# Kernel optimization log

Measured on AMD Instinct MI355X. Metric: run time of the kernel, lower is better.

The kernel has to match this reference:

```python
import jax, jax.numpy as jnp
import numpy as np

B, N, DIM = 4, 1024, 512
H, DH = 8, 64
INNER = H * DH
MLP = 2048
EPS = 1e-5


def layernorm(x, g, b):
    m = x.mean(-1, keepdims=True)
    v = ((x - m) ** 2).mean(-1, keepdims=True)
    return (x - m) / jnp.sqrt(v + EPS) * g + b


def setup_inputs() -> dict:
    key = jax.random.key(0)
    ks = jax.random.split(key, 12)
    s = 0.02
    return {
        "q": jax.random.normal(ks[0], (B, N, DIM), jnp.float32),
        "k": jax.random.normal(ks[1], (B, N, DIM), jnp.float32),
        "v": jax.random.normal(ks[2], (B, N, DIM), jnp.float32),
        "Win": jax.random.normal(ks[3], (INNER, DIM), jnp.float32) * s,
        "Wout": jax.random.normal(ks[4], (DIM, INNER), jnp.float32) * s,
        "bout": jnp.zeros((DIM,), jnp.float32),
        "g1": jnp.ones((DIM,), jnp.float32),
        "b1n": jnp.zeros((DIM,), jnp.float32),
        "g2": jnp.ones((DIM,), jnp.float32),
        "b2n": jnp.zeros((DIM,), jnp.float32),
        "Wup": jax.random.normal(ks[5], (MLP, DIM), jnp.float32) * s,
        "bup": jnp.zeros((MLP,), jnp.float32),
        "Wdn": jax.random.normal(ks[6], (DIM, MLP), jnp.float32) * s,
        "bdn": jnp.zeros((DIM,), jnp.float32),
        "wp_W1": jax.random.normal(ks[7], (DH, 2 * DH), jnp.float32) * s,
        "wp_b1": jnp.zeros((DH,), jnp.float32),
        "wp_g": jnp.ones((DH,), jnp.float32),
        "wp_b": jnp.zeros((DH,), jnp.float32),
        "wp_W2": jax.random.normal(ks[8], (3, DH), jnp.float32) * s,
        "wp_b2": jnp.zeros((3,), jnp.float32),
        "num_heads": H,
        "dim_head": DH,
        "mlp_dim": MLP,
    }


def reference(q, k, v, Win, Wout, bout, g1, b1n, g2, b2n, Wup, bup, Wdn, bdn,
              wp_W1, wp_b1, wp_g, wp_b, wp_W2, wp_b2, num_heads, dim_head, mlp_dim):
    b, n, _ = q.shape

    def split_heads(x):  # [b,n,dim] -> [h,b,n,d]
        f = x @ Win.T
        return f.reshape(b, n, num_heads, dim_head).transpose(2, 0, 1, 3)

    fq = split_heads(layernorm(q, g1, b1n))
    fk = split_heads(layernorm(k, g1, b1n))
    fv = split_heads(layernorm(v, g1, b1n))

    # cosine similarity component
    dots = jnp.einsum('hbnd,hbmd->hbnm', fq, fk)
    nq = jnp.linalg.norm(fq, axis=-1)  # [h,b,n]
    nk = jnp.linalg.norm(fk, axis=-1)  # [h,b,m]
    cosine_sim = dots / (nq[..., :, None] * nk[..., None, :])

    # mean-centered covariance component
    qc = fq - fq.mean(-1, keepdims=True)
    kc = fk - fk.mean(-1, keepdims=True)
    cov_component = jnp.einsum('hbnd,hbmd->hbnm', qc, kc) / dim_head

    # variance outer-product component (torch.var -> unbiased, ddof=1)
    qv = jnp.var(fq, axis=-1, ddof=1)  # [h,b,n]
    kv = jnp.var(fk, axis=-1, ddof=1)  # [h,b,m]
    var_component = qv[..., :, None] * kv[..., None, :] / dim_head

    # dynamic per-head mixing weights
    qg = fq.mean(axis=(1, 2))  # [h,d]
    kg = fk.mean(axis=(1, 2))
    feats = jnp.concatenate([qg, kg], axis=-1)  # [h,2d]
    h1 = jax.nn.relu(layernorm(feats @ wp_W1.T + wp_b1, wp_g, wp_b))
    w = jax.nn.softmax(h1 @ wp_W2.T + wp_b2, axis=-1)  # [h,3]
    cw = w[:, 0][:, None, None, None]
    covw = w[:, 1][:, None, None, None]
    vw = w[:, 2][:, None, None, None]

    scores = cw * cosine_sim + covw * cov_component + vw * var_component
    out = jnp.einsum('hbnm,hbmd->hbnd', scores, fv)
    out = out.transpose(1, 2, 0, 3).reshape(b, n, num_heads * dim_head)
    attn = out @ Wout.T + bout

    q2 = q + attn
    x = layernorm(q2, g2, b2n)
    y = jax.nn.gelu(x @ Wup.T + bup, approximate=False) @ Wdn.T + bdn
    return q2 + y
```

## Files before the change

### kernel.cpp

```cpp
#include <hip/hip_runtime.h>
#include <math.h>

#define EPS 1e-5f
#define ROWS 4096

typedef __attribute__((ext_vector_type(8))) short short8;
typedef __attribute__((ext_vector_type(4))) float floatx4;

__device__ inline short f2bf(float f) {
    unsigned u = __builtin_bit_cast(unsigned, f);
    unsigned r = (u + 0x7fffu + ((u >> 16) & 1u)) >> 16;
    return (short)r;
}

__global__ __launch_bounds__(256) void lnconv(
    const float* __restrict__ x0, const float* __restrict__ x1,
    const float* __restrict__ x2, const float* __restrict__ g,
    const float* __restrict__ bb, short* __restrict__ out) {
    int tensor = blockIdx.y;
    const float* x = tensor == 0 ? x0 : (tensor == 1 ? x1 : x2);
    int t = threadIdx.x;
    int row = blockIdx.x * 4 + (t >> 6);
    int col = (t & 63) * 8;
    const float* xr = x + (size_t)row * 512 + col;
    float4 v0 = *(const float4*)xr;
    float4 v1 = *(const float4*)(xr + 4);
    float s = v0.x + v0.y + v0.z + v0.w + v1.x + v1.y + v1.z + v1.w;
    float sq = v0.x * v0.x + v0.y * v0.y + v0.z * v0.z + v0.w * v0.w +
               v1.x * v1.x + v1.y * v1.y + v1.z * v1.z + v1.w * v1.w;
#pragma unroll
    for (int off = 32; off; off >>= 1) {
        s += __shfl_xor(s, off);
        sq += __shfl_xor(sq, off);
    }
    float m = s * (1.f / 512.f);
    float rstd = rsqrtf(sq * (1.f / 512.f) - m * m + EPS);
    float4 g0 = *(const float4*)(g + col);
    float4 g1 = *(const float4*)(g + col + 4);
    float4 b0 = *(const float4*)(bb + col);
    float4 b1 = *(const float4*)(bb + col + 4);
    short8 o;
    o[0] = f2bf((v0.x - m) * rstd * g0.x + b0.x);
    o[1] = f2bf((v0.y - m) * rstd * g0.y + b0.y);
    o[2] = f2bf((v0.z - m) * rstd * g0.z + b0.z);
    o[3] = f2bf((v0.w - m) * rstd * g0.w + b0.w);
    o[4] = f2bf((v1.x - m) * rstd * g1.x + b1.x);
    o[5] = f2bf((v1.y - m) * rstd * g1.y + b1.y);
    o[6] = f2bf((v1.z - m) * rstd * g1.z + b1.z);
    o[7] = f2bf((v1.w - m) * rstd * g1.w + b1.w);
    *(short8*)(out + (size_t)(tensor * 4096 + row) * 512 + col) = o;
}

__global__ void wconv(const float* __restrict__ w0, const float* __restrict__ w1,
                      const float* __restrict__ w2, const float* __restrict__ w3,
                      short* __restrict__ o0, short* __restrict__ o1,
                      short* __restrict__ o2, short* __restrict__ o3,
                      float* __restrict__ qgz) {
    int y = blockIdx.y;
    if (y == 0) {
        int zi = blockIdx.x * 256 + threadIdx.x;
        if (zi < 1024) qgz[zi] = 0.f;
    }
    const float* src = y == 0 ? w0 : (y == 1 ? w1 : (y == 2 ? w2 : w3));
    short* dst = y == 0 ? o0 : (y == 1 ? o1 : (y == 2 ? o2 : o3));
    int n = (y < 2) ? 262144 : 1048576;
    int idx = (blockIdx.x * 256 + threadIdx.x) * 8;
    if (idx < n) {
        float4 v0 = *(const float4*)(src + idx);
        float4 v1 = *(const float4*)(src + idx + 4);
        short8 o;
        o[0] = f2bf(v0.x); o[1] = f2bf(v0.y); o[2] = f2bf(v0.z); o[3] = f2bf(v0.w);
        o[4] = f2bf(v1.x); o[5] = f2bf(v1.y); o[6] = f2bf(v1.z); o[7] = f2bf(v1.w);
        *(short8*)(dst + idx) = o;
    }
}

template <int TM, int TN, int EPI, bool OUT_BF16>
__global__ __launch_bounds__(256) void mfma_gemm_nt(
    const short* __restrict__ A, const short* __restrict__ B,
    void* __restrict__ C, int M, int N, int K,
    const float* __restrict__ bias, const float* __restrict__ resid) {
    constexpr int FI = TM / 32;
    constexpr int FJ = TN / 32;
    __shared__ short As[TM * 32];
    __shared__ short Bs[TN * 32];
    int t = threadIdx.x;
    int m0 = blockIdx.y * TM, n0 = blockIdx.x * TN;
    int w = t >> 6, lane = t & 63;
    int wm = (w & 1) * (TM / 2), wn = (w >> 1) * (TN / 2);
    floatx4 acc[FI][FJ];
#pragma unroll
    for (int i = 0; i < FI; ++i)
#pragma unroll
        for (int j = 0; j < FJ; ++j) acc[i][j] = (floatx4){0.f, 0.f, 0.f, 0.f};

    int arow = t >> 2, acol = (t & 3) * 8;
    const short* Ag = A + (size_t)(m0 + arow) * K + acol;
    const short* Bg = B + (size_t)(n0 + arow) * K + acol;
    int ldsbase = w * 1024;

    for (int k0 = 0; k0 < K; k0 += 32) {
        __syncthreads();
#pragma unroll
        for (int u = 0; u < TM / 64; ++u)
            __builtin_amdgcn_global_load_lds(
                (const __attribute__((address_space(1))) void*)(Ag + (size_t)u * 64 * K + k0),
                (__attribute__((address_space(3))) void*)((char*)As + u * 4096 + ldsbase),
                16, 0, 0);
#pragma unroll
        for (int u = 0; u < TN / 64; ++u)
            __builtin_amdgcn_global_load_lds(
                (const __attribute__((address_space(1))) void*)(Bg + (size_t)u * 64 * K + k0),
                (__attribute__((address_space(3))) void*)((char*)Bs + u * 4096 + ldsbase),
                16, 0, 0);
        __syncthreads();
        int krow = (lane >> 4) * 8;
        short8 af[FI], bf[FJ];
#pragma unroll
        for (int i = 0; i < FI; ++i)
            af[i] = *(const short8*)&As[(wm + i * 16 + (lane & 15)) * 32 + krow];
#pragma unroll
        for (int j = 0; j < FJ; ++j)
            bf[j] = *(const short8*)&Bs[(wn + j * 16 + (lane & 15)) * 32 + krow];
#pragma unroll
        for (int i = 0; i < FI; ++i)
#pragma unroll
            for (int j = 0; j < FJ; ++j)
                acc[i][j] = __builtin_amdgcn_mfma_f32_16x16x32_bf16(
                    af[i], bf[j], acc[i][j], 0, 0, 0);
    }

    int col = lane & 15, rbase = (lane >> 4) * 4;
#pragma unroll
    for (int i = 0; i < FI; ++i) {
#pragma unroll
        for (int j = 0; j < FJ; ++j) {
            int gcol = n0 + wn + j * 16 + col;
#pragma unroll
            for (int r = 0; r < 4; ++r) {
                int grow = m0 + wm + i * 16 + rbase + r;
                float v = acc[i][j][r];
                if (EPI == 2) v += bias[gcol] + resid[(size_t)grow * N + gcol];
                if (EPI == 3) {
                    v += bias[gcol];
                    v = 0.5f * v * (1.f + erff(v * 0.70710678118654752f));
                }
                if (OUT_BF16)
                    ((short*)C)[(size_t)grow * N + gcol] = f2bf(v);
                else
                    ((float*)C)[(size_t)grow * N + gcol] = v;
            }
        }
    }
}

__global__ __launch_bounds__(512) void stats_fused(
    const float* __restrict__ fq, const float* __restrict__ fk,
    float* __restrict__ S, float* __restrict__ qg, float* __restrict__ kg) {
    int y = blockIdx.y;
    const float* f = y ? fk : fq;
    float* base = S + (size_t)y * 98304;
    float* o = y ? kg : qg;
    int t = threadIdx.x;
    int h = t >> 6, lane = t & 63;
    int r0 = blockIdx.x * 32;
    float csum = 0.f;
    for (int r = 0; r < 32; ++r) {
        float v = f[(size_t)(r0 + r) * 512 + t];
        csum += v;
        float s = v, sq = v * v;
#pragma unroll
        for (int off = 32; off; off >>= 1) {
            s += __shfl_xor(s, off);
            sq += __shfl_xor(sq, off);
        }
        if (lane == 0) {
            float m = s * (1.f / 64.f);
            int idx = h * ROWS + r0 + r;
            base[idx] = m;
            base[32768 + idx] = rsqrtf(sq);
            base[65536 + idx] = (sq - 64.f * m * m) * (1.f / 63.f);
        }
    }
    atomicAdd(&o[t], csum * (1.f / 4096.f));
}

__global__ void policy_mlp(const float* __restrict__ qg, const float* __restrict__ kg,
                           const float* __restrict__ W1, const float* __restrict__ b1,
                           const float* __restrict__ g, const float* __restrict__ bb,
                           const float* __restrict__ W2, const float* __restrict__ b2,
                           float* __restrict__ wmix) {
    int h = blockIdx.x, j = threadIdx.x;
    float acc = 0.f;
    const float* w1r = W1 + j * 128;
    for (int i = 0; i < 64; ++i) acc += qg[h * 64 + i] * w1r[i];
    for (int i = 0; i < 64; ++i) acc += kg[h * 64 + i] * w1r[64 + i];
    acc += b1[j];
    float s = acc, sq = acc * acc;
#pragma unroll
    for (int off = 32; off; off >>= 1) {
        s += __shfl_xor(s, off);
        sq += __shfl_xor(sq, off);
    }
    float m = s * (1.f / 64.f);
    float var = sq * (1.f / 64.f) - m * m;
    float xh = (acc - m) * rsqrtf(var + EPS) * g[j] + bb[j];
    float r = fmaxf(xh, 0.f);
    float l[3];
#pragma unroll
    for (int c = 0; c < 3; ++c) {
        float p = r * W2[c * 64 + j];
#pragma unroll
        for (int off = 32; off; off >>= 1) p += __shfl_xor(p, off);
        l[c] = p + b2[c];
    }
    if (j == 0) {
        float mx = fmaxf(l[0], fmaxf(l[1], l[2]));
        float e0 = expf(l[0] - mx), e1 = expf(l[1] - mx), e2 = expf(l[2] - mx);
        float inv = 1.f / (e0 + e1 + e2);
        wmix[h * 3 + 0] = e0 * inv;
        wmix[h * 3 + 1] = e1 * inv;
        wmix[h * 3 + 2] = e2 * inv;
    }
}

__global__ __launch_bounds__(256) void ksideP(
    const float* __restrict__ fk, const float* __restrict__ fv,
    const float* __restrict__ rnk, const float* __restrict__ kvv,
    const float* __restrict__ mk, float* __restrict__ Mpart) {
    int hb = blockIdx.x;
    int chunk = blockIdx.y;
    int h = hb >> 2, b = hb & 3;
    __shared__ float fkt[2048], fvt[2048];
    __shared__ float rs[32], kvs[32], mks[32];
    int t = threadIdx.x;
    int td = t >> 4, te = t & 15;
    float m1[4][4] = {}, m2[4][4] = {};
    float skv = 0.f, smk = 0.f;
    int mstart = chunk * 128;
    for (int m0 = mstart; m0 < mstart + 128; m0 += 32) {
        __syncthreads();
#pragma unroll
        for (int u = 0; u < 2; ++u) {
            int idx = u * 1024 + t * 4;
            int mm = idx >> 6, d = idx & 63;
            size_t grow = (size_t)(b * 1024 + m0 + mm) * 512 + h * 64 + d;
            *(float4*)&fkt[idx] = *(const float4*)&fk[grow];
            *(float4*)&fvt[idx] = *(const float4*)&fv[grow];
        }
        if (t < 32) {
            int sidx = h * ROWS + b * 1024 + m0 + t;
            rs[t] = rnk[sidx];
            kvs[t] = kvv[sidx];
            mks[t] = mk[sidx];
        }
        __syncthreads();
        for (int mi = 0; mi < 32; ++mi) {
            float r = rs[mi];
            float4 kq = *(const float4*)&fkt[mi * 64 + td * 4];
            float4 vq = *(const float4*)&fvt[mi * 64 + te * 4];
            float kr[4] = {kq.x, kq.y, kq.z, kq.w};
            float vr[4] = {vq.x, vq.y, vq.z, vq.w};
#pragma unroll
            for (int i = 0; i < 4; ++i) {
                float kv_ = kr[i], krr = kv_ * r;
#pragma unroll
                for (int j = 0; j < 4; ++j) {
                    m2[i][j] += kv_ * vr[j];
                    m1[i][j] += krr * vr[j];
                }
            }
            if (t < 64) {
                skv += kvs[mi] * fvt[mi * 64 + t];
                smk += mks[mi] * fvt[mi * 64 + t];
            }
        }
    }
    float* base = Mpart + (size_t)(chunk * 32 + hb) * 8320;
#pragma unroll
    for (int i = 0; i < 4; ++i)
#pragma unroll
        for (int j = 0; j < 4; ++j) {
            base[(td * 4 + i) * 64 + te * 4 + j] = m1[i][j];
            base[4096 + (td * 4 + i) * 64 + te * 4 + j] = m2[i][j];
        }
    if (t < 64) {
        base[8192 + t] = skv;
        base[8256 + t] = smk;
    }
}

__global__ void reduceM(const float* __restrict__ Mpart, float* __restrict__ Mbuf) {
    int i = blockIdx.x * 256 + threadIdx.x;
    if (i < 32 * 8320) {
        float s = 0.f;
#pragma unroll
        for (int c = 0; c < 8; ++c) s += Mpart[(size_t)c * 266240 + i];
        Mbuf[i] = s;
    }
}

__global__ __launch_bounds__(256) void qside(
    const float* __restrict__ fq, const float* __restrict__ Mbuf,
    const float* __restrict__ rnq, const float* __restrict__ mq,
    const float* __restrict__ qv, const float* __restrict__ wmix,
    short* __restrict__ attn_out) {
    int ntile = blockIdx.x, hb = blockIdx.y;
    int h = hb >> 2, b = hb & 3;
    __shared__ float M1s[4096], M2s[4096], fqt[4096];
    __shared__ float Skvs[64], Smks[64], rnqs[64], mqs[64], qvs[64];
    int t = threadIdx.x;
    const float* base = Mbuf + (size_t)hb * 8320;
#pragma unroll
    for (int u = 0; u < 4; ++u) {
        int idx = t * 4 + u * 1024;
        *(float4*)&M1s[idx] = *(const float4*)&base[idx];
        *(float4*)&M2s[idx] = *(const float4*)&base[4096 + idx];
    }
    int n0 = ntile * 64;
#pragma unroll
    for (int u = 0; u < 4; ++u) {
        int idx = t * 4 + u * 1024;
        int r = idx >> 6, d = idx & 63;
        *(float4*)&fqt[idx] = *(const float4*)&fq[(size_t)(b * 1024 + n0 + r) * 512 + h * 64 + d];
    }
    if (t < 64) {
        Skvs[t] = base[8192 + t];
        Smks[t] = base[8256 + t];
        int sidx = h * ROWS + b * 1024 + n0 + t;
        rnqs[t] = rnq[sidx];
        mqs[t] = mq[sidx];
        qvs[t] = qv[sidx];
    }
    __syncthreads();
    float cw = wmix[h * 3 + 0], covw = wmix[h * 3 + 1], vw = wmix[h * 3 + 2];
    int e = t & 63, rq = t >> 6;
    float a1[16] = {}, a2[16] = {};
    for (int d4 = 0; d4 < 64; d4 += 4) {
        float md1[4], md2[4];
#pragma unroll
        for (int dd = 0; dd < 4; ++dd) {
            md1[dd] = M1s[(d4 + dd) * 64 + e];
            md2[dd] = M2s[(d4 + dd) * 64 + e];
        }
#pragma unroll
        for (int i = 0; i < 16; ++i) {
            float4 f = *(const float4*)&fqt[(rq * 16 + i) * 64 + d4];
            a1[i] += f.x * md1[0] + f.y * md1[1] + f.z * md1[2] + f.w * md1[3];
            a2[i] += f.x * md2[0] + f.y * md2[1] + f.z * md2[2] + f.w * md2[3];
        }
    }
    float c2 = covw * (1.f / 64.f), c3 = vw * (1.f / 64.f);
#pragma unroll
    for (int i = 0; i < 16; ++i) {
        int rr = rq * 16 + i;
        float v = cw * rnqs[rr] * a1[i] + c2 * a2[i] + c3 * qvs[rr] * Skvs[e] -
                  covw * mqs[rr] * Smks[e];
        attn_out[(size_t)(b * 1024 + n0 + rr) * 512 + h * 64 + e] = f2bf(v);
    }
}

extern "C" void kernel_launch(void* const* d_in, const int* in_sizes, int n_in,
                              void* d_out, int out_size, void* d_ws, size_t ws_size,
                              hipStream_t stream) {
    const float* q = (const float*)d_in[0];
    const float* k = (const float*)d_in[1];
    const float* v = (const float*)d_in[2];
    const float* Win = (const float*)d_in[3];
    const float* Wout = (const float*)d_in[4];
    const float* bout = (const float*)d_in[5];
    const float* g1 = (const float*)d_in[6];
    const float* b1n = (const float*)d_in[7];
    const float* g2 = (const float*)d_in[8];
    const float* b2n = (const float*)d_in[9];
    const float* Wup = (const float*)d_in[10];
    const float* bup = (const float*)d_in[11];
    const float* Wdn = (const float*)d_in[12];
    const float* bdn = (const float*)d_in[13];
    const float* wpW1 = (const float*)d_in[14];
    const float* wpb1 = (const float*)d_in[15];
    const float* wpg = (const float*)d_in[16];
    const float* wpb = (const float*)d_in[17];
    const float* wpW2 = (const float*)d_in[18];
    const float* wpb2 = (const float*)d_in[19];
    float* out = (float*)d_out;

    float* wsf = (float*)d_ws;
    float* fq = wsf;
    float* fk = wsf + 2097152;
    float* fv = wsf + 2 * 2097152;
    short* hmid = (short*)wsf;
    short* qkvln = (short*)(wsf + 6291456);
    float* Mpart = wsf + 6291456;
    short* attnbf = (short*)(wsf + 6291456);
    short* x2bf = (short*)(wsf + 6291456 + 1048576);
    short* Winbf = (short*)(wsf + 9437184);
    short* Woutbf = (short*)(wsf + 9437184 + 131072);
    short* Wupbf = (short*)(wsf + 9437184 + 262144);
    short* Wdnbf = (short*)(wsf + 9437184 + 262144 + 524288);
    float* S = wsf + 10747904;
    float* qg = S + 196608;
    float* kg = qg + 512;
    float* Mbuf = kg + 512;
    float* wmix = Mbuf + 266240;
    float* mqS = S, *rnqS = S + 32768, *qvS = S + 65536;
    float* mkS = S + 98304, *rnkS = S + 131072, *kvS = S + 163840;

    wconv<<<dim3(512, 4), 256, 0, stream>>>(Win, Wout, Wup, Wdn,
                                            Winbf, Woutbf, Wupbf, Wdnbf, qg);
    lnconv<<<dim3(1024, 3), 256, 0, stream>>>(q, k, v, g1, b1n, qkvln);

    mfma_gemm_nt<128, 128, 0, false><<<dim3(4, 96), 256, 0, stream>>>(
        qkvln, Winbf, fq, 12288, 512, 512, nullptr, nullptr);

    stats_fused<<<dim3(128, 2), 512, 0, stream>>>(fq, fk, S, qg, kg);
    policy_mlp<<<8, 64, 0, stream>>>(qg, kg, wpW1, wpb1, wpg, wpb, wpW2, wpb2, wmix);

    ksideP<<<dim3(32, 8), 256, 0, stream>>>(fk, fv, rnkS, kvS, mkS, Mpart);
    reduceM<<<1040, 256, 0, stream>>>(Mpart, Mbuf);
    qside<<<dim3(16, 32), 256, 0, stream>>>(fq, Mbuf, rnqS, mqS, qvS, wmix, attnbf);

    mfma_gemm_nt<64, 128, 2, false><<<dim3(4, 64), 256, 0, stream>>>(
        attnbf, Woutbf, out, 4096, 512, 512, bout, q);

    lnconv<<<dim3(1024, 1), 256, 0, stream>>>(out, out, out, g2, b2n, x2bf);
    mfma_gemm_nt<128, 128, 3, true><<<dim3(16, 32), 256, 0, stream>>>(
        x2bf, Wupbf, hmid, 4096, 2048, 512, bup, nullptr);
    mfma_gemm_nt<64, 128, 2, false><<<dim3(4, 64), 256, 0, stream>>>(
        hmid, Wdnbf, out, 4096, 512, 2048, bdn, out);
}
```

Baseline: 283.8 us.

## Fuse prep kernels, stats into QKV GEMM epilogue, and atomics replacing reduceM

Merges the weight conversion, layernorm conversion and buffer zeroing into one prep kernel. Per-head row statistics and column means move into the QKV projection GEMM epilogue, which removes the separate stats pass over fq/fk. The policy MLP becomes an extra block column of ksideP, and partial M sums are atomically added into Mbuf, so reduceM is no longer needed. GEMM tile sizes shrink (64x128, 64x64) to launch more blocks. The trade is more atomic traffic and possible ordering concerns: the policy block reads qg/kg in the same launch, which is fine because the GEMM wrote them earlier.

```diff
diff --git a/kernel.cpp b/kernel.cpp
--- a/kernel.cpp
+++ b/kernel.cpp
@@ -13,12 +13,210 @@
     return (short)r;
 }
 
+__global__ __launch_bounds__(256) void prep(
+    const float* __restrict__ q, const float* __restrict__ k,
+    const float* __restrict__ v, const float* __restrict__ g,
+    const float* __restrict__ bb, short* __restrict__ qkvout,
+    const float* __restrict__ w0, const float* __restrict__ w1,
+    const float* __restrict__ w2, const float* __restrict__ w3,
+    short* __restrict__ o0, short* __restrict__ o1,
+    short* __restrict__ o2, short* __restrict__ o3,
+    float* __restrict__ zero0) {
+    int bx = blockIdx.x;
+    int t = threadIdx.x;
+    if (bx < 3072) {
+        int tensor = bx >> 10;
+        int xb = bx & 1023;
+        const float* x = tensor == 0 ? q : (tensor == 1 ? k : v);
+        int row = xb * 4 + (t >> 6);
+        int col = (t & 63) * 8;
+        const float* xr = x + (size_t)row * 512 + col;
+        float4 v0 = *(const float4*)xr;
+        float4 v1 = *(const float4*)(xr + 4);
+        float s = v0.x + v0.y + v0.z + v0.w + v1.x + v1.y + v1.z + v1.w;
+        float sq = v0.x * v0.x + v0.y * v0.y + v0.z * v0.z + v0.w * v0.w +
+                   v1.x * v1.x + v1.y * v1.y + v1.z * v1.z + v1.w * v1.w;
+#pragma unroll
+        for (int off = 32; off; off >>= 1) {
+            s += __shfl_xor(s, off);
+            sq += __shfl_xor(sq, off);
+        }
+        float m = s * (1.f / 512.f);
+        float rstd = rsqrtf(sq * (1.f / 512.f) - m * m + EPS);
+        float4 g0 = *(const float4*)(g + col);
+        float4 g1 = *(const float4*)(g + col + 4);
+        float4 b0 = *(const float4*)(bb + col);
+        float4 b1 = *(const float4*)(bb + col + 4);
+        short8 o;
+        o[0] = f2bf((v0.x - m) * rstd * g0.x + b0.x);
+        o[1] = f2bf((v0.y - m) * rstd * g0.y + b0.y);
+        o[2] = f2bf((v0.z - m) * rstd * g0.z + b0.z);
+        o[3] = f2bf((v0.w - m) * rstd * g0.w + b0.w);
+        o[4] = f2bf((v1.x - m) * rstd * g1.x + b1.x);
+        o[5] = f2bf((v1.y - m) * rstd * g1.y + b1.y);
+        o[6] = f2bf((v1.z - m) * rstd * g1.z + b1.z);
+        o[7] = f2bf((v1.w - m) * rstd * g1.w + b1.w);
+        *(short8*)(qkvout + (size_t)(tensor * 4096 + row) * 512 + col) = o;
+        return;
+    }
+    if (bx < 4352) {
+        int wb = bx - 3072;
+        const float* src;
+        short* dst;
+        int base;
+        if (wb < 128) { src = w0; dst = o0; base = wb; }
+        else if (wb < 256) { src = w1; dst = o1; base = wb - 128; }
+        else if (wb < 768) { src = w2; dst = o2; base = wb - 256; }
+        else { src = w3; dst = o3; base = wb - 768; }
+        int idx = base * 2048 + t * 8;
+        float4 v0 = *(const float4*)(src + idx);
+        float4 v1 = *(const float4*)(src + idx + 4);
+        short8 o;
+        o[0] = f2bf(v0.x); o[1] = f2bf(v0.y); o[2] = f2bf(v0.z); o[3] = f2bf(v0.w);
+        o[4] = f2bf(v1.x); o[5] = f2bf(v1.y); o[6] = f2bf(v1.z); o[7] = f2bf(v1.w);
+        *(short8*)(dst + idx) = o;
+        return;
+    }
+    int zi = (bx - 4352) * 1024 + t * 4;
+    if (zi < 267264) *(float4*)(zero0 + zi) = (float4){0.f, 0.f, 0.f, 0.f};
+}
+
+template <int TM, int TN, int EPI, bool OUT_BF16>
+__global__ __launch_bounds__(256) void mfma_gemm_nt(
+    const short* __restrict__ A, const short* __restrict__ B,
+    void* __restrict__ C, int M, int N, int K,
+    const float* __restrict__ bias, const float* __restrict__ resid,
+    float* __restrict__ Sb, float* __restrict__ qgp, float* __restrict__ kgp) {
+    constexpr int FI = TM / 32;
+    constexpr int FJ = TN / 32;
+    __shared__ short As[TM * 32];
+    __shared__ short Bs[TN * 32];
+    int t = threadIdx.x;
+    int m0 = blockIdx.y * TM, n0 = blockIdx.x * TN;
+    int w = t >> 6, lane = t & 63;
+    int wm = (w & 1) * (TM / 2), wn = (w >> 1) * (TN / 2);
+    floatx4 acc[FI][FJ];
+#pragma unroll
+    for (int i = 0; i < FI; ++i)
+#pragma unroll
+        for (int j = 0; j < FJ; ++j) acc[i][j] = (floatx4){0.f, 0.f, 0.f, 0.f};
+
+    int arow = t >> 2, acol = (t & 3) * 8;
+    const short* Ag = A + (size_t)(m0 + arow) * K + acol;
+    const short* Bg = B + (size_t)(n0 + arow) * K + acol;
+    int ldsbase = w * 1024;
+
+    for (int k0 = 0; k0 < K; k0 += 32) {
+        __syncthreads();
+#pragma unroll
+        for (int u = 0; u < TM / 64; ++u)
+            __builtin_amdgcn_global_load_lds(
+                (const __attribute__((address_space(1))) void*)(Ag + (size_t)u * 64 * K + k0),
+                (__attribute__((address_space(3))) void*)((char*)As + u * 4096 + ldsbase),
+                16, 0, 0);
+#pragma unroll
+        for (int u = 0; u < TN / 64; ++u)
+            __builtin_amdgcn_global_load_lds(
+                (const __attribute__((address_space(1))) void*)(Bg + (size_t)u * 64 * K + k0),
+                (__attribute__((address_space(3))) void*)((char*)Bs + u * 4096 + ldsbase),
+                16, 0, 0);
+        __syncthreads();
+        int krow = (lane >> 4) * 8;
+        short8 af[FI], bf[FJ];
+#pragma unroll
+        for (int i = 0; i < FI; ++i)
+            af[i] = *(const short8*)&As[(wm + i * 16 + (lane & 15)) * 32 + krow];
+#pragma unroll
+        for (int j = 0; j < FJ; ++j)
+            bf[j] = *(const short8*)&Bs[(wn + j * 16 + (lane & 15)) * 32 + krow];
+#pragma unroll
+        for (int i = 0; i < FI; ++i)
+#pragma unroll
+            for (int j = 0; j < FJ; ++j)
+                acc[i][j] = __builtin_amdgcn_mfma_f32_16x16x32_bf16(
+                    af[i], bf[j], acc[i][j], 0, 0, 0);
+    }
+
+    int col = lane & 15, rbase = (lane >> 4) * 4;
+#pragma unroll
+    for (int i = 0; i < FI; ++i) {
+#pragma unroll
+        for (int j = 0; j < FJ; ++j) {
+            int gcol = n0 + wn + j * 16 + col;
+#pragma unroll
+            for (int r = 0; r < 4; ++r) {
+                int grow = m0 + wm + i * 16 + rbase + r;
+                float v = acc[i][j][r];
+                if (EPI == 2) v += bias[gcol] + resid[(size_t)grow * N + gcol];
+                if (EPI == 3) {
+                    v += bias[gcol];
+                    v = 0.5f * v * (1.f + erff(v * 0.70710678118654752f));
+                }
+                if (OUT_BF16)
+                    ((short*)C)[(size_t)grow * N + gcol] = f2bf(v);
+                else
+                    ((float*)C)[(size_t)grow * N + gcol] = v;
+            }
+        }
+    }
+
+    if (EPI == 1) {
+        if (m0 < 8192) {
+            int tensor = m0 >> 12;
+            float* Sbase = Sb + (size_t)tensor * 98304;
+            float* dst = tensor ? kgp : qgp;
+            int head = (n0 + wn) >> 6;
+            int rowbase = (m0 & 4095) + wm;
+#pragma unroll
+            for (int i = 0; i < FI; ++i) {
+#pragma unroll
+                for (int r = 0; r < 4; ++r) {
+                    float s = 0.f, sq = 0.f;
+#pragma unroll
+                    for (int j = 0; j < FJ; ++j) {
+                        float vv = acc[i][j][r];
+                        s += vv;
+                        sq += vv * vv;
+                    }
+#pragma unroll
+                    for (int off = 1; off < 16; off <<= 1) {
+                        s += __shfl_xor(s, off);
+                        sq += __shfl_xor(sq, off);
+                    }
+                    if ((lane & 15) == 0) {
+                        int row = rowbase + i * 16 + rbase + r;
+                        int idx = head * ROWS + row;
+                        float m = s * (1.f / 64.f);
+                        Sbase[idx] = m;
+                        Sbase[32768 + idx] = rsqrtf(sq);
+                        Sbase[65536 + idx] = (sq - 64.f * m * m) * (1.f / 63.f);
+                    }
+                }
+            }
+            float cs[FJ];
+#pragma unroll
+            for (int j = 0; j < FJ; ++j) {
+                float s = 0.f;
+#pragma unroll
+                for (int i = 0; i < FI; ++i)
+#pragma unroll
+                    for (int r = 0; r < 4; ++r) s += acc[i][j][r];
+                s += __shfl_xor(s, 16);
+                s += __shfl_xor(s, 32);
+                cs[j] = s;
+            }
+            if (lane < 16) {
+#pragma unroll
+                for (int j = 0; j < FJ; ++j)
+                    atomicAdd(&dst[head * 64 + j * 16 + lane], cs[j] * (1.f / 4096.f));
+            }
+        }
+    }
+}
+
 __global__ __launch_bounds__(256) void lnconv(
-    const float* __restrict__ x0, const float* __restrict__ x1,
-    const float* __restrict__ x2, const float* __restrict__ g,
+    const float* __restrict__ x, const float* __restrict__ g,
     const float* __restrict__ bb, short* __restrict__ out) {
-    int tensor = blockIdx.y;
-    const float* x = tensor == 0 ? x0 : (tensor == 1 ? x1 : x2);
     int t = threadIdx.x;
     int row = blockIdx.x * 4 + (t >> 6);
     int col = (t & 63) * 8;
@@ -48,186 +246,55 @@
     o[5] = f2bf((v1.y - m) * rstd * g1.y + b1.y);
     o[6] = f2bf((v1.z - m) * rstd * g1.z + b1.z);
     o[7] = f2bf((v1.w - m) * rstd * g1.w + b1.w);
-    *(short8*)(out + (size_t)(tensor * 4096 + row) * 512 + col) = o;
-}
-
-__global__ void wconv(const float* __restrict__ w0, const float* __restrict__ w1,
-                      const float* __restrict__ w2, const float* __restrict__ w3,
-                      short* __restrict__ o0, short* __restrict__ o1,
-                      short* __restrict__ o2, short* __restrict__ o3,
-                      float* __restrict__ qgz) {
-    int y = blockIdx.y;
-    if (y == 0) {
-        int zi = blockIdx.x * 256 + threadIdx.x;
-        if (zi < 1024) qgz[zi] = 0.f;
-    }
-    const float* src = y == 0 ? w0 : (y == 1 ? w1 : (y == 2 ? w2 : w3));
-    short* dst = y == 0 ? o0 : (y == 1 ? o1 : (y == 2 ? o2 : o3));
-    int n = (y < 2) ? 262144 : 1048576;
-    int idx = (blockIdx.x * 256 + threadIdx.x) * 8;
-    if (idx < n) {
-        float4 v0 = *(const float4*)(src + idx);
-        float4 v1 = *(const float4*)(src + idx + 4);
-        short8 o;
-        o[0] = f2bf(v0.x); o[1] = f2bf(v0.y); o[2] = f2bf(v0.z); o[3] = f2bf(v0.w);
-        o[4] = f2bf(v1.x); o[5] = f2bf(v1.y); o[6] = f2bf(v1.z); o[7] = f2bf(v1.w);
-        *(short8*)(dst + idx) = o;
-    }
-}
-
-template <int TM, int TN, int EPI, bool OUT_BF16>
-__global__ __launch_bounds__(256) void mfma_gemm_nt(
-    const short* __restrict__ A, const short* __restrict__ B,
-    void* __restrict__ C, int M, int N, int K,
-    const float* __restrict__ bias, const float* __restrict__ resid) {
-    constexpr int FI = TM / 32;
-    constexpr int FJ = TN / 32;
-    __shared__ short As[TM * 32];
-    __shared__ short Bs[TN * 32];
-    int t = threadIdx.x;
-    int m0 = blockIdx.y * TM, n0 = blockIdx.x * TN;
-    int w = t >> 6, lane = t & 63;
-    int wm = (w & 1) * (TM / 2), wn = (w >> 1) * (TN / 2);
-    floatx4 acc[FI][FJ];
-#pragma unroll
-    for (int i = 0; i < FI; ++i)
-#pragma unroll
-        for (int j = 0; j < FJ; ++j) acc[i][j] = (floatx4){0.f, 0.f, 0.f, 0.f};
-
-    int arow = t >> 2, acol = (t & 3) * 8;
-    const short* Ag = A + (size_t)(m0 + arow) * K + acol;
-    const short* Bg = B + (size_t)(n0 + arow) * K + acol;
-    int ldsbase = w * 1024;
-
-    for (int k0 = 0; k0 < K; k0 += 32) {
-        __syncthreads();
-#pragma unroll
-        for (int u = 0; u < TM / 64; ++u)
-            __builtin_amdgcn_global_load_lds(
-                (const __attribute__((address_space(1))) void*)(Ag + (size_t)u * 64 * K + k0),
-                (__attribute__((address_space(3))) void*)((char*)As + u * 4096 + ldsbase),
-                16, 0, 0);
-#pragma unroll
-        for (int u = 0; u < TN / 64; ++u)
-            __builtin_amdgcn_global_load_lds(
-                (const __attribute__((address_space(1))) void*)(Bg + (size_t)u * 64 * K + k0),
-                (__attribute__((address_space(3))) void*)((char*)Bs + u * 4096 + ldsbase),
-                16, 0, 0);
-        __syncthreads();
-        int krow = (lane >> 4) * 8;
-        short8 af[FI], bf[FJ];
-#pragma unroll
-        for (int i = 0; i < FI; ++i)
-            af[i] = *(const short8*)&As[(wm + i * 16 + (lane & 15)) * 32 + krow];
-#pragma unroll
-        for (int j = 0; j < FJ; ++j)
-            bf[j] = *(const short8*)&Bs[(wn + j * 16 + (lane & 15)) * 32 + krow];
-#pragma unroll
-        for (int i = 0; i < FI; ++i)
-#pragma unroll
-            for (int j = 0; j < FJ; ++j)
-                acc[i][j] = __builtin_amdgcn_mfma_f32_16x16x32_bf16(
-                    af[i], bf[j], acc[i][j], 0, 0, 0);
-    }
-
-    int col = lane & 15, rbase = (lane >> 4) * 4;
-#pragma unroll
-    for (int i = 0; i < FI; ++i) {
-#pragma unroll
-        for (int j = 0; j < FJ; ++j) {
-            int gcol = n0 + wn + j * 16 + col;
-#pragma unroll
-            for (int r = 0; r < 4; ++r) {
-                int grow = m0 + wm + i * 16 + rbase + r;
-                float v = acc[i][j][r];
-                if (EPI == 2) v += bias[gcol] + resid[(size_t)grow * N + gcol];
-                if (EPI == 3) {
-                    v += bias[gcol];
-                    v = 0.5f * v * (1.f + erff(v * 0.70710678118654752f));
-                }
-                if (OUT_BF16)
-                    ((short*)C)[(size_t)grow * N + gcol] = f2bf(v);
-                else
-                    ((float*)C)[(size_t)grow * N + gcol] = v;
-            }
-        }
-    }
-}
-
-__global__ __launch_bounds__(512) void stats_fused(
-    const float* __restrict__ fq, const float* __restrict__ fk,
-    float* __restrict__ S, float* __restrict__ qg, float* __restrict__ kg) {
-    int y = blockIdx.y;
-    const float* f = y ? fk : fq;
-    float* base = S + (size_t)y * 98304;
-    float* o = y ? kg : qg;
-    int t = threadIdx.x;
-    int h = t >> 6, lane = t & 63;
-    int r0 = blockIdx.x * 32;
-    float csum = 0.f;
-    for (int r = 0; r < 32; ++r) {
-        float v = f[(size_t)(r0 + r) * 512 + t];
-        csum += v;
-        float s = v, sq = v * v;
+    *(short8*)(out + (size_t)row * 512 + col) = o;
+}
+
+__global__ __launch_bounds__(256) void ksideP(
+    const float* __restrict__ fk, const float* __restrict__ fv,
+    const float* __restrict__ rnk, const float* __restrict__ kvv,
+    const float* __restrict__ mk, float* __restrict__ Mbuf,
+    const float* __restrict__ qg, const float* __restrict__ kg,
+    const float* __restrict__ W1, const float* __restrict__ b1,
+    const float* __restrict__ g, const float* __restrict__ bb,
+    const float* __restrict__ W2, const float* __restrict__ b2,
+    float* __restrict__ wmix) {
+    if (blockIdx.x == 32) {
+        int j = threadIdx.x;
+        if (j >= 64) return;
+        int h = blockIdx.y;
+        float acc = 0.f;
+        const float* w1r = W1 + j * 128;
+        for (int i = 0; i < 64; ++i) acc += qg[h * 64 + i] * w1r[i];
+        for (int i = 0; i < 64; ++i) acc += kg[h * 64 + i] * w1r[64 + i];
+        acc += b1[j];
+        float s = acc, sq = acc * acc;
 #pragma unroll
         for (int off = 32; off; off >>= 1) {
             s += __shfl_xor(s, off);
             sq += __shfl_xor(sq, off);
         }
-        if (lane == 0) {
-            float m = s * (1.f / 64.f);
-            int idx = h * ROWS + r0 + r;
-            base[idx] = m;
-            base[32768 + idx] = rsqrtf(sq);
-            base[65536 + idx] = (sq - 64.f * m * m) * (1.f / 63.f);
-        }
-    }
-    atomicAdd(&o[t], csum * (1.f / 4096.f));
-}
-
-__global__ void policy_mlp(const float* __restrict__ qg, const float* __restrict__ kg,
-                           const float* __restrict__ W1, const float* __restrict__ b1,
-                           const float* __restrict__ g, const float* __restrict__ bb,
-                           const float* __restrict__ W2, const float* __restrict__ b2,
-                           float* __restrict__ wmix) {
-    int h = blockIdx.x, j = threadIdx.x;
-    float acc = 0.f;
-    const float* w1r = W1 + j * 128;
-    for (int i = 0; i < 64; ++i) acc += qg[h * 64 + i] * w1r[i];
-    for (int i = 0; i < 64; ++i) acc += kg[h * 64 + i] * w1r[64 + i];
-    acc += b1[j];
-    float s = acc, sq = acc * acc;
-#pragma unroll
-    for (int off = 32; off; off >>= 1) {
-        s += __shfl_xor(s, off);
-        sq += __shfl_xor(sq, off);
-    }
-    float m = s * (1.f / 64.f);
-    float var = sq * (1.f / 64.f) - m * m;
-    float xh = (acc - m) * rsqrtf(var + EPS) * g[j] + bb[j];
-    float r = fmaxf(xh, 0.f);
-    float l[3];
-#pragma unroll
-    for (int c = 0; c < 3; ++c) {
-        float p = r * W2[c * 64 + j];
-#pragma unroll
-        for (int off = 32; off; off >>= 1) p += __shfl_xor(p, off);
-        l[c] = p + b2[c];
-    }
-    if (j == 0) {
-        float mx = fmaxf(l[0], fmaxf(l[1], l[2]));
-        float e0 = expf(l[0] - mx), e1 = expf(l[1] - mx), e2 = expf(l[2] - mx);
-        float inv = 1.f / (e0 + e1 + e2);
-        wmix[h * 3 + 0] = e0 * inv;
-        wmix[h * 3 + 1] = e1 * inv;
-        wmix[h * 3 + 2] = e2 * inv;
-    }
-}
-
-__global__ __launch_bounds__(256) void ksideP(
-    const float* __restrict__ fk, const float* __restrict__ fv,
-    const float* __restrict__ rnk, const float* __restrict__ kvv,
-    const float* __restrict__ mk, float* __restrict__ Mpart) {
+        float m = s * (1.f / 64.f);
+        float var = sq * (1.f / 64.f) - m * m;
+        float xh = (acc - m) * rsqrtf(var + EPS) * g[j] + bb[j];
+        float r = fmaxf(xh, 0.f);
+        float l[3];
+#pragma unroll
+        for (int c = 0; c < 3; ++c) {
+            float p = r * W2[c * 64 + j];
+#pragma unroll
+            for (int off = 32; off; off >>= 1) p += __shfl_xor(p, off);
+            l[c] = p + b2[c];
+        }
+        if (j == 0) {
+            float mx = fmaxf(l[0], fmaxf(l[1], l[2]));
+            float e0 = expf(l[0] - mx), e1 = expf(l[1] - mx), e2 = expf(l[2] - mx);
+            float inv = 1.f / (e0 + e1 + e2);
+            wmix[h * 3 + 0] = e0 * inv;
+            wmix[h * 3 + 1] = e1 * inv;
+            wmix[h * 3 + 2] = e2 * inv;
+        }
+        return;
+    }
     int hb = blockIdx.x;
     int chunk = blockIdx.y;
     int h = hb >> 2, b = hb & 3;
@@ -276,27 +343,17 @@
             }
         }
     }
-    float* base = Mpart + (size_t)(chunk * 32 + hb) * 8320;
+    float* base = Mbuf + (size_t)hb * 8320;
 #pragma unroll
     for (int i = 0; i < 4; ++i)
 #pragma unroll
         for (int j = 0; j < 4; ++j) {
-            base[(td * 4 + i) * 64 + te * 4 + j] = m1[i][j];
-            base[4096 + (td * 4 + i) * 64 + te * 4 + j] = m2[i][j];
+            atomicAdd(&base[(td * 4 + i) * 64 + te * 4 + j], m1[i][j]);
+            atomicAdd(&base[4096 + (td * 4 + i) * 64 + te * 4 + j], m2[i][j]);
         }
     if (t < 64) {
-        base[8192 + t] = skv;
-        base[8256 + t] = smk;
-    }
-}
-
-__global__ void reduceM(const float* __restrict__ Mpart, float* __restrict__ Mbuf) {
-    int i = blockIdx.x * 256 + threadIdx.x;
-    if (i < 32 * 8320) {
-        float s = 0.f;
-#pragma unroll
-        for (int c = 0; c < 8; ++c) s += Mpart[(size_t)c * 266240 + i];
-        Mbuf[i] = s;
+        atomicAdd(&base[8192 + t], skv);
+        atomicAdd(&base[8256 + t], smk);
     }
 }
 
@@ -391,7 +448,6 @@
     float* fv = wsf + 2 * 2097152;
     short* hmid = (short*)wsf;
     short* qkvln = (short*)(wsf + 6291456);
-    float* Mpart = wsf + 6291456;
     short* attnbf = (short*)(wsf + 6291456);
     short* x2bf = (short*)(wsf + 6291456 + 1048576);
     short* Winbf = (short*)(wsf + 9437184);
@@ -406,26 +462,25 @@
     float* mqS = S, *rnqS = S + 32768, *qvS = S + 65536;
     float* mkS = S + 98304, *rnkS = S + 131072, *kvS = S + 163840;
 
-    wconv<<<dim3(512, 4), 256, 0, stream>>>(Win, Wout, Wup, Wdn,
-                                            Winbf, Woutbf, Wupbf, Wdnbf, qg);
-    lnconv<<<dim3(1024, 3), 256, 0, stream>>>(q, k, v, g1, b1n, qkvln);
-
-    mfma_gemm_nt<128, 128, 0, false><<<dim3(4, 96), 256, 0, stream>>>(
-        qkvln, Winbf, fq, 12288, 512, 512, nullptr, nullptr);
-
-    stats_fused<<<dim3(128, 2), 512, 0, stream>>>(fq, fk, S, qg, kg);
-    policy_mlp<<<8, 64, 0, stream>>>(qg, kg, wpW1, wpb1, wpg, wpb, wpW2, wpb2, wmix);
-
-    ksideP<<<dim3(32, 8), 256, 0, stream>>>(fk, fv, rnkS, kvS, mkS, Mpart);
-    reduceM<<<1040, 256, 0, stream>>>(Mpart, Mbuf);
+    prep<<<4613, 256, 0, stream>>>(q, k, v, g1, b1n, qkvln,
+                                   Win, Wout, Wup, Wdn,
+                                   Winbf, Woutbf, Wupbf, Wdnbf, qg);
+
+    mfma_gemm_nt<64, 128, 1, false><<<dim3(4, 192), 256, 0, stream>>>(
+        qkvln, Winbf, fq, 12288, 512, 512, nullptr, nullptr, S, qg, kg);
+
+    ksideP<<<dim3(33, 8), 256, 0, stream>>>(fk, fv, rnkS, kvS, mkS, Mbuf,
+                                            qg, kg, wpW1, wpb1, wpg, wpb,
+                                            wpW2, wpb2, wmix);
+
     qside<<<dim3(16, 32), 256, 0, stream>>>(fq, Mbuf, rnqS, mqS, qvS, wmix, attnbf);
 
+    mfma_gemm_nt<64, 64, 2, false><<<dim3(8, 64), 256, 0, stream>>>(
+        attnbf, Woutbf, out, 4096, 512, 512, bout, q, nullptr, nullptr, nullptr);
+
+    lnconv<<<1024, 256, 0, stream>>>(out, g2, b2n, x2bf);
+    mfma_gemm_nt<64, 128, 3, true><<<dim3(16, 64), 256, 0, stream>>>(
+        x2bf, Wupbf, hmid, 4096, 2048, 512, bup, nullptr, nullptr, nullptr, nullptr);
     mfma_gemm_nt<64, 128, 2, false><<<dim3(4, 64), 256, 0, stream>>>(
-        attnbf, Woutbf, out, 4096, 512, 512, bout, q);
-
-    lnconv<<<dim3(1024, 1), 256, 0, stream>>>(out, out, out, g2, b2n, x2bf);
-    mfma_gemm_nt<128, 128, 3, true><<<dim3(16, 32), 256, 0, stream>>>(
-        x2bf, Wupbf, hmid, 4096, 2048, 512, bup, nullptr);
-    mfma_gemm_nt<64, 128, 2, false><<<dim3(4, 64), 256, 0, stream>>>(
-        hmid, Wdnbf, out, 4096, 512, 2048, bdn, out);
-}
+        hmid, Wdnbf, out, 4096, 512, 2048, bdn, out, nullptr, nullptr, nullptr);
+}
```

Result: faster. 274.2 us (-3.4%).
